# Optimization experiments

Hardware: AMD Instinct MI355X
Metric: run time of the kernel (lower is better)

## Reference

```python
import jax, jax.numpy as jnp
import numpy as np

C = 64
DQ = C // 8  # query/key channel dim


def setup_inputs() -> dict:
    key = jax.random.key(0)
    ks = jax.random.split(key, 8)
    B, H, W = 8, 64, 64
    x = jax.random.normal(ks[0], (B, C, H, W), dtype=jnp.float32)
    # 1x1 conv weights stored as [out, in] matrices (kernel dims squeezed)
    wq = jax.random.normal(ks[1], (DQ, C), dtype=jnp.float32) * 0.05
    bq = jax.random.normal(ks[2], (DQ,), dtype=jnp.float32) * 0.05
    wk = jax.random.normal(ks[3], (DQ, C), dtype=jnp.float32) * 0.05
    bk = jax.random.normal(ks[4], (DQ,), dtype=jnp.float32) * 0.05
    wv = jax.random.normal(ks[5], (C, C), dtype=jnp.float32) * 0.05
    bv = jax.random.normal(ks[6], (C,), dtype=jnp.float32) * 0.05
    gamma = jax.random.normal(ks[7], (1,), dtype=jnp.float32)
    return {"x": x, "wq": wq, "bq": bq, "wk": wk, "bk": bk,
            "wv": wv, "bv": bv, "gamma": gamma}


def reference(x, wq, bq, wk, bk, wv, bv, gamma):
    B, Cc, H, W = x.shape
    N = H * W
    xf = x.reshape(B, Cc, N)                      # [B, C, N]
    # 1x1 convs == channel matmuls
    q = jnp.einsum('dc,bcn->bdn', wq, xf) + bq[None, :, None]   # [B, DQ, N]
    k = jnp.einsum('dc,bcn->bdn', wk, xf) + bk[None, :, None]   # [B, DQ, N]
    v = jnp.einsum('oc,bcn->bon', wv, xf) + bv[None, :, None]   # [B, C, N]
    # energy[b, m, n] = sum_d q[b, d, m] * k[b, d, n]
    energy = jnp.einsum('bdm,bdn->bmn', q, k)                   # [B, N, N]
    attention = jax.nn.softmax(energy, axis=-1)
    # out[b, c, m] = sum_n v[b, c, n] * attention[b, m, n]
    out = jnp.einsum('bcn,bmn->bcm', v, attention).reshape(B, Cc, H, W)
    return gamma[0] * out + x
```

## Files before the change

kernel.cpp:

```cpp
#include <hip/hip_runtime.h>
#include <math.h>

#define NTOK 4096
#define CCH  64
#define LOG2E 1.4426950408889634f

typedef __attribute__((ext_vector_type(8)))  short bf16x8;
typedef __attribute__((ext_vector_type(4)))  float f32x4;
typedef __attribute__((ext_vector_type(16))) float f32x16;
typedef __attribute__((ext_vector_type(2)))  unsigned int uint32x2;

__device__ __forceinline__ unsigned short f2bf_rne(float f) {
    unsigned int u = __float_as_uint(f);
    u += 0x7FFFu + ((u >> 16) & 1u);
    return (unsigned short)(u >> 16);
}
__device__ __forceinline__ unsigned short f2bf_trunc(float f) {
    return (unsigned short)(__float_as_uint(f) >> 16);
}
__device__ __forceinline__ float bf2f(unsigned short u) {
    return __uint_as_float(((unsigned int)u) << 16);
}

__global__ __launch_bounds__(256) void proj_kernel(
    const float* __restrict__ x,
    const float* __restrict__ wq, const float* __restrict__ bq,
    const float* __restrict__ wk, const float* __restrict__ bk,
    const float* __restrict__ wv, const float* __restrict__ bv,
    unsigned short* __restrict__ qt, unsigned short* __restrict__ kt,
    unsigned short* __restrict__ vbf)
{
    __shared__ unsigned short xsb[64 * 68];
    __shared__ unsigned short wa[80 * 68];
    __shared__ unsigned short vtmp[64 * 66];
    __shared__ float bb[80];

    const int t  = threadIdx.x;
    const int b  = blockIdx.x >> 6;
    const int n0 = (blockIdx.x & 63) << 6;

    const int lane = t & 63;
    const int w    = t >> 6;
    const int l15  = lane & 15;
    const int g    = lane >> 4;

    {
        const int n  = t & 63;
        const int c0 = t >> 6;
        #pragma unroll
        for (int r = 0; r < 16; ++r) {
            const int c = c0 + 4 * r;
            xsb[n * 68 + c] = f2bf_rne(x[((size_t)(b * CCH + c)) * NTOK + n0 + n]);
        }
    }
    #pragma unroll
    for (int r = 0; r < 16; ++r) {
        const int i = t + 256 * r;
        wa[(i >> 6) * 68 + (i & 63)] = f2bf_rne(wv[i]);
    }
    {
        const int i0 = t, i1 = t + 256;
        wa[(64 + (i0 >> 6)) * 68 + (i0 & 63)] = f2bf_rne(wq[i0] * LOG2E);
        wa[(64 + (i1 >> 6)) * 68 + (i1 & 63)] = f2bf_rne(wq[i1] * LOG2E);
        wa[(72 + (i0 >> 6)) * 68 + (i0 & 63)] = f2bf_rne(wk[i0]);
        wa[(72 + (i1 >> 6)) * 68 + (i1 & 63)] = f2bf_rne(wk[i1]);
    }
    if (t < 80) {
        float bias;
        if (t < 64)      bias = bv[t];
        else if (t < 72) bias = bq[t - 64] * LOG2E;
        else             bias = bk[t - 72];
        bb[t] = bias;
    }
    __syncthreads();

    f32x4 acc[5];
    #pragma unroll
    for (int mt = 0; mt < 5; ++mt) acc[mt] = (f32x4){0.f, 0.f, 0.f, 0.f};
    #pragma unroll
    for (int kc = 0; kc < 2; ++kc) {
        const bf16x8 bx = *(const bf16x8*)&xsb[(w * 16 + l15) * 68 + kc * 32 + g * 8];
        #pragma unroll
        for (int mt = 0; mt < 5; ++mt) {
            const bf16x8 aw = *(const bf16x8*)&wa[(mt * 16 + l15) * 68 + kc * 32 + g * 8];
            acc[mt] = __builtin_amdgcn_mfma_f32_16x16x32_bf16(aw, bx, acc[mt], 0, 0, 0);
        }
    }

    const int n = w * 16 + l15;
    #pragma unroll
    for (int mt = 0; mt < 4; ++mt) {
        #pragma unroll
        for (int r = 0; r < 4; ++r) {
            const int c = mt * 16 + g * 4 + r;
            vtmp[c * 66 + 4 * l15 + w] = f2bf_rne(acc[mt][r] + bb[c]);
        }
    }
    {
        unsigned short vals[4];
        #pragma unroll
        for (int r = 0; r < 4; ++r)
            vals[r] = f2bf_rne(acc[4][r] + bb[64 + g * 4 + r]);
        const unsigned int lo = (unsigned int)vals[0] | ((unsigned int)vals[1] << 16);
        const unsigned int hi = (unsigned int)vals[2] | ((unsigned int)vals[3] << 16);
        unsigned short* dst = ((g < 2) ? qt : kt) +
                              ((size_t)(b * NTOK + n0 + n)) * 8 + (g & 1) * 4;
        *(uint32x2*)dst = (uint32x2){lo, hi};
    }
    __syncthreads();

    {
        const int c = t >> 2;
        const int q = t & 3;
        unsigned short* dst = vbf + ((size_t)(b * CCH + c)) * NTOK + n0 + q * 16;
        *(bf16x8*)dst       = *(const bf16x8*)&vtmp[c * 66 + q * 16];
        *(bf16x8*)(dst + 8) = *(const bf16x8*)&vtmp[c * 66 + q * 16 + 8];
    }
}

__global__ __launch_bounds__(256, 4) void attn_kernel(
    const unsigned short* __restrict__ qt, const unsigned short* __restrict__ kt,
    const unsigned short* __restrict__ vbf,
    unsigned short* __restrict__ opart, float* __restrict__ lpart)
{
    __shared__ unsigned short qs[64 * 32];
    __shared__ unsigned short ks[64 * 40];
    __shared__ unsigned short vs[64 * 88];
    __shared__ unsigned short ps[64 * 88];

    const int t    = threadIdx.x;
    const int lane = t & 63;
    const int w    = t >> 6;
    const int p    = blockIdx.x >> 9;
    const int rest = blockIdx.x & 511;
    const int b    = rest >> 6;
    const int m0   = (rest & 63) << 6;

    const int l15 = lane & 15;
    const int g   = lane >> 4;
    const int l31 = lane & 31;
    const int h   = lane >> 5;

    if (t < 64) {
        *(bf16x8*)&qs[t * 32] = *(const bf16x8*)&qt[((size_t)(b * NTOK + m0 + t)) * 8];
        bf16x8 z = {};
        *(bf16x8*)&qs[t * 32 + 8]  = z;
        *(bf16x8*)&qs[t * 32 + 16] = z;
        *(bf16x8*)&qs[t * 32 + 24] = z;
        *(bf16x8*)&ks[t * 40 + 8]  = z;
        *(bf16x8*)&ks[t * 40 + 16] = z;
        *(bf16x8*)&ks[t * 40 + 24] = z;
    }
    __syncthreads();

    const bf16x8 a_q = *(const bf16x8*)&qs[(w * 16 + l15) * 32 + g * 8];

    f32x16 oacc;
    #pragma unroll
    for (int i = 0; i < 16; ++i) oacc[i] = 0.f;
    float rs0 = 0.f, rs1 = 0.f, rs2 = 0.f, rs3 = 0.f;

    const int crow = ((w >> 1) * 32 + l31) * 88;
    const int mrow = ((w & 1) * 32 + l31) * 88;

    for (int it = p * 32; it < p * 32 + 32; ++it) {
        const int nt0 = it << 6;
        __syncthreads();

        if (t < 64)
            *(bf16x8*)&ks[t * 40] = *(const bf16x8*)&kt[((size_t)(b * NTOK + nt0 + t)) * 8];
        #pragma unroll
        for (int r = 0; r < 2; ++r) {
            const int i   = t + 256 * r;
            const int c   = i >> 3;
            const int seg = i & 7;
            *(bf16x8*)&vs[c * 88 + seg * 8] =
                *(const bf16x8*)&vbf[((size_t)(b * CCH + c)) * NTOK + nt0 + seg * 8];
        }
        __syncthreads();

        f32x4 s0, s1, s2, s3;
        {
            const bf16x8 bk0 = *(const bf16x8*)&ks[( 0 + l15) * 40 + g * 8];
            const bf16x8 bk1 = *(const bf16x8*)&ks[(16 + l15) * 40 + g * 8];
            const bf16x8 bk2 = *(const bf16x8*)&ks[(32 + l15) * 40 + g * 8];
            const bf16x8 bk3 = *(const bf16x8*)&ks[(48 + l15) * 40 + g * 8];
            const f32x4 z = {0.f, 0.f, 0.f, 0.f};
            s0 = __builtin_amdgcn_mfma_f32_16x16x32_bf16(a_q, bk0, z, 0, 0, 0);
            s1 = __builtin_amdgcn_mfma_f32_16x16x32_bf16(a_q, bk1, z, 0, 0, 0);
            s2 = __builtin_amdgcn_mfma_f32_16x16x32_bf16(a_q, bk2, z, 0, 0, 0);
            s3 = __builtin_amdgcn_mfma_f32_16x16x32_bf16(a_q, bk3, z, 0, 0, 0);
        }

        #pragma unroll
        for (int r = 0; r < 4; ++r) {
            const float p0 = exp2f(s0[r]);
            const float p1 = exp2f(s1[r]);
            const float p2 = exp2f(s2[r]);
            const float p3 = exp2f(s3[r]);
            const unsigned int lo = (unsigned int)f2bf_trunc(p0) |
                                    ((unsigned int)f2bf_trunc(p1) << 16);
            const unsigned int hi = (unsigned int)f2bf_trunc(p2) |
                                    ((unsigned int)f2bf_trunc(p3) << 16);
            *(uint32x2*)&ps[(w * 16 + g * 4 + r) * 88 + 4 * l15] = (uint32x2){lo, hi};
            const float ssum = (p0 + p1) + (p2 + p3);
            if      (r == 0) rs0 += ssum;
            else if (r == 1) rs1 += ssum;
            else if (r == 2) rs2 += ssum;
            else             rs3 += ssum;
        }
        __syncthreads();

        #pragma unroll
        for (int kc = 0; kc < 4; ++kc) {
            const bf16x8 a_v = *(const bf16x8*)&vs[crow + kc * 16 + h * 8];
            const bf16x8 b_p = *(const bf16x8*)&ps[mrow + kc * 16 + h * 8];
            oacc = __builtin_amdgcn_mfma_f32_32x32x16_bf16(a_v, b_p, oacc, 0, 0, 0);
        }
    }

    #pragma unroll
    for (int xm = 1; xm <= 8; xm <<= 1) {
        rs0 += __shfl_xor(rs0, xm);
        rs1 += __shfl_xor(rs1, xm);
        rs2 += __shfl_xor(rs2, xm);
        rs3 += __shfl_xor(rs3, xm);
    }
    if (l15 == 0) {
        float* lp = lpart + (size_t)(p * 8 + b) * NTOK + m0 + w * 16 + g * 4;
        lp[0] = rs0; lp[1] = rs1; lp[2] = rs2; lp[3] = rs3;
    }

    {
        const int mloc = (w & 1) * 32 + l31;
        #pragma unroll
        for (int reg = 0; reg < 16; ++reg) {
            const int c = (w >> 1) * 32 + (reg & 3) + 8 * (reg >> 2) + 4 * h;
            opart[((size_t)((p * 8 + b) * CCH + c)) * NTOK + m0 + mloc] =
                f2bf_rne(oacc[reg]);
        }
    }
}

__global__ __launch_bounds__(256) void combine_kernel(
    const unsigned short* __restrict__ opart, const float* __restrict__ lpart,
    const float* __restrict__ x, const float* __restrict__ gamma_p,
    float* __restrict__ out)
{
    const size_t idx = (size_t)blockIdx.x * 256 + threadIdx.x;
    const int m4 = ((int)idx & 1023) * 4;
    const int bc = (int)(idx >> 10);
    const int bi = bc >> 6;

    const size_t obase   = (size_t)bc * NTOK + m4;
    const size_t ostride = (size_t)8 * CCH * NTOK;

    const ushort4 o1 = *(const ushort4*)&opart[obase];
    const ushort4 o2 = *(const ushort4*)&opart[obase + ostride];
    const float4  l1 = *(const float4*)&lpart[(size_t)bi * NTOK + m4];
    const float4  l2 = *(const float4*)&lpart[(size_t)(8 + bi) * NTOK + m4];
    const float4  xv = *(const float4*)&x[obase];
    const float   gm = gamma_p[0];

    float4 r;
    r.x = (bf2f(o1.x) + bf2f(o2.x)) * gm / (l1.x + l2.x) + xv.x;
    r.y = (bf2f(o1.y) + bf2f(o2.y)) * gm / (l1.y + l2.y) + xv.y;
    r.z = (bf2f(o1.z) + bf2f(o2.z)) * gm / (l1.z + l2.z) + xv.z;
    r.w = (bf2f(o1.w) + bf2f(o2.w)) * gm / (l1.w + l2.w) + xv.w;
    *(float4*)&out[obase] = r;
}

extern "C" void kernel_launch(void* const* d_in, const int* in_sizes, int n_in,
                              void* d_out, int out_size, void* d_ws, size_t ws_size,
                              hipStream_t stream) {
    const float* x     = (const float*)d_in[0];
    const float* wq    = (const float*)d_in[1];
    const float* bq    = (const float*)d_in[2];
    const float* wk    = (const float*)d_in[3];
    const float* bk    = (const float*)d_in[4];
    const float* wv    = (const float*)d_in[5];
    const float* bv    = (const float*)d_in[6];
    const float* gamma = (const float*)d_in[7];
    float* out = (float*)d_out;

    const int B = in_sizes[0] / (CCH * NTOK);

    unsigned short* wsp   = (unsigned short*)d_ws;
    unsigned short* qt    = wsp;
    unsigned short* kt    = qt + (size_t)B * NTOK * 8;
    unsigned short* vbf   = kt + (size_t)B * NTOK * 8;
    unsigned short* opart = vbf + (size_t)B * CCH * NTOK;
    float*          lpart = (float*)(opart + (size_t)2 * B * CCH * NTOK);

    proj_kernel<<<B * (NTOK / 64), 256, 0, stream>>>(x, wq, bq, wk, bk, wv, bv,
                                                     qt, kt, vbf);
    attn_kernel<<<2 * B * (NTOK / 64), 256, 0, stream>>>(qt, kt, vbf, opart, lpart);
    combine_kernel<<<(B * CCH * NTOK) / (256 * 4), 256, 0, stream>>>(
        opart, lpart, x, gamma, out);
}
```

Before: 135.7 us.

## Fuse projection, attention and combine into one cooperative persistent kernel

Merges the three kernels into one cooperative launch. Blocks loop over projection tiles, attention tiles and combine elements, with grid.sync between the phases, and the two shared-memory layouts are unioned. The goal is to remove the launch overhead and inter-kernel gaps between the three stages. In exchange it adds host-side occupancy queries on every call, grid-wide barriers, and a grid capped by occupancy, so attention tiles may run in uneven waves. It falls back to the three separate kernels if the cooperative launch fails.

After: 445.9 us. 3.29x slower.

```diff
diff --git a/kernel.cpp b/kernel.cpp
--- a/kernel.cpp
+++ b/kernel.cpp
@@ -1,5 +1,8 @@
 #include <hip/hip_runtime.h>
+#include <hip/hip_cooperative_groups.h>
 #include <math.h>
+
+namespace cg = cooperative_groups;
 
 #define NTOK 4096
 #define CCH  64
@@ -22,7 +25,21 @@
     return __uint_as_float(((unsigned int)u) << 16);
 }
 
-__global__ __launch_bounds__(256) void proj_kernel(
+struct ProjS {
+    unsigned short xsb[64 * 68];
+    unsigned short wa[80 * 68];
+    unsigned short vtmp[64 * 66];
+    float bb[80];
+};
+struct AttnS {
+    unsigned short qs[64 * 32];
+    unsigned short ks[64 * 40];
+    unsigned short vs[64 * 88];
+    unsigned short ps[64 * 88];
+};
+
+__device__ __forceinline__ void proj_tile(
+    ProjS& s, int vb, int t,
     const float* __restrict__ x,
     const float* __restrict__ wq, const float* __restrict__ bq,
     const float* __restrict__ wk, const float* __restrict__ bk,
@@ -30,15 +47,8 @@
     unsigned short* __restrict__ qt, unsigned short* __restrict__ kt,
     unsigned short* __restrict__ vbf)
 {
-    __shared__ unsigned short xsb[64 * 68];
-    __shared__ unsigned short wa[80 * 68];
-    __shared__ unsigned short vtmp[64 * 66];
-    __shared__ float bb[80];
-
-    const int t  = threadIdx.x;
-    const int b  = blockIdx.x >> 6;
-    const int n0 = (blockIdx.x & 63) << 6;
-
+    const int b  = vb >> 6;
+    const int n0 = (vb & 63) << 6;
     const int lane = t & 63;
     const int w    = t >> 6;
     const int l15  = lane & 15;
@@ -50,27 +60,27 @@
         #pragma unroll
         for (int r = 0; r < 16; ++r) {
             const int c = c0 + 4 * r;
-            xsb[n * 68 + c] = f2bf_rne(x[((size_t)(b * CCH + c)) * NTOK + n0 + n]);
+            s.xsb[n * 68 + c] = f2bf_rne(x[((size_t)(b * CCH + c)) * NTOK + n0 + n]);
         }
     }
     #pragma unroll
     for (int r = 0; r < 16; ++r) {
         const int i = t + 256 * r;
-        wa[(i >> 6) * 68 + (i & 63)] = f2bf_rne(wv[i]);
+        s.wa[(i >> 6) * 68 + (i & 63)] = f2bf_rne(wv[i]);
     }
     {
         const int i0 = t, i1 = t + 256;
-        wa[(64 + (i0 >> 6)) * 68 + (i0 & 63)] = f2bf_rne(wq[i0] * LOG2E);
-        wa[(64 + (i1 >> 6)) * 68 + (i1 & 63)] = f2bf_rne(wq[i1] * LOG2E);
-        wa[(72 + (i0 >> 6)) * 68 + (i0 & 63)] = f2bf_rne(wk[i0]);
-        wa[(72 + (i1 >> 6)) * 68 + (i1 & 63)] = f2bf_rne(wk[i1]);
+        s.wa[(64 + (i0 >> 6)) * 68 + (i0 & 63)] = f2bf_rne(wq[i0] * LOG2E);
+        s.wa[(64 + (i1 >> 6)) * 68 + (i1 & 63)] = f2bf_rne(wq[i1] * LOG2E);
+        s.wa[(72 + (i0 >> 6)) * 68 + (i0 & 63)] = f2bf_rne(wk[i0]);
+        s.wa[(72 + (i1 >> 6)) * 68 + (i1 & 63)] = f2bf_rne(wk[i1]);
     }
     if (t < 80) {
         float bias;
         if (t < 64)      bias = bv[t];
         else if (t < 72) bias = bq[t - 64] * LOG2E;
         else             bias = bk[t - 72];
-        bb[t] = bias;
+        s.bb[t] = bias;
     }
     __syncthreads();
 
@@ -79,10 +89,10 @@
     for (int mt = 0; mt < 5; ++mt) acc[mt] = (f32x4){0.f, 0.f, 0.f, 0.f};
     #pragma unroll
     for (int kc = 0; kc < 2; ++kc) {
-        const bf16x8 bx = *(const bf16x8*)&xsb[(w * 16 + l15) * 68 + kc * 32 + g * 8];
+        const bf16x8 bx = *(const bf16x8*)&s.xsb[(w * 16 + l15) * 68 + kc * 32 + g * 8];
         #pragma unroll
         for (int mt = 0; mt < 5; ++mt) {
-            const bf16x8 aw = *(const bf16x8*)&wa[(mt * 16 + l15) * 68 + kc * 32 + g * 8];
+            const bf16x8 aw = *(const bf16x8*)&s.wa[(mt * 16 + l15) * 68 + kc * 32 + g * 8];
             acc[mt] = __builtin_amdgcn_mfma_f32_16x16x32_bf16(aw, bx, acc[mt], 0, 0, 0);
         }
     }
@@ -93,14 +103,14 @@
         #pragma unroll
         for (int r = 0; r < 4; ++r) {
             const int c = mt * 16 + g * 4 + r;
-            vtmp[c * 66 + 4 * l15 + w] = f2bf_rne(acc[mt][r] + bb[c]);
+            s.vtmp[c * 66 + 4 * l15 + w] = f2bf_rne(acc[mt][r] + s.bb[c]);
         }
     }
     {
         unsigned short vals[4];
         #pragma unroll
         for (int r = 0; r < 4; ++r)
-            vals[r] = f2bf_rne(acc[4][r] + bb[64 + g * 4 + r]);
+            vals[r] = f2bf_rne(acc[4][r] + s.bb[64 + g * 4 + r]);
         const unsigned int lo = (unsigned int)vals[0] | ((unsigned int)vals[1] << 16);
         const unsigned int hi = (unsigned int)vals[2] | ((unsigned int)vals[3] << 16);
         unsigned short* dst = ((g < 2) ? qt : kt) +
@@ -113,47 +123,42 @@
         const int c = t >> 2;
         const int q = t & 3;
         unsigned short* dst = vbf + ((size_t)(b * CCH + c)) * NTOK + n0 + q * 16;
-        *(bf16x8*)dst       = *(const bf16x8*)&vtmp[c * 66 + q * 16];
-        *(bf16x8*)(dst + 8) = *(const bf16x8*)&vtmp[c * 66 + q * 16 + 8];
-    }
-}
-
-__global__ __launch_bounds__(256, 4) void attn_kernel(
+        *(bf16x8*)dst       = *(const bf16x8*)&s.vtmp[c * 66 + q * 16];
+        *(bf16x8*)(dst + 8) = *(const bf16x8*)&s.vtmp[c * 66 + q * 16 + 8];
+    }
+}
+
+__device__ __forceinline__ void attn_tile(
+    AttnS& s, int vb, int t, int B,
     const unsigned short* __restrict__ qt, const unsigned short* __restrict__ kt,
     const unsigned short* __restrict__ vbf,
     unsigned short* __restrict__ opart, float* __restrict__ lpart)
 {
-    __shared__ unsigned short qs[64 * 32];
-    __shared__ unsigned short ks[64 * 40];
-    __shared__ unsigned short vs[64 * 88];
-    __shared__ unsigned short ps[64 * 88];
-
-    const int t    = threadIdx.x;
+    const int p    = vb / (B * 64);
+    const int rest = vb % (B * 64);
+    const int b    = rest >> 6;
+    const int m0   = (rest & 63) << 6;
+
     const int lane = t & 63;
     const int w    = t >> 6;
-    const int p    = blockIdx.x >> 9;
-    const int rest = blockIdx.x & 511;
-    const int b    = rest >> 6;
-    const int m0   = (rest & 63) << 6;
-
-    const int l15 = lane & 15;
-    const int g   = lane >> 4;
-    const int l31 = lane & 31;
-    const int h   = lane >> 5;
+    const int l15  = lane & 15;
+    const int g    = lane >> 4;
+    const int l31  = lane & 31;
+    const int h    = lane >> 5;
 
     if (t < 64) {
-        *(bf16x8*)&qs[t * 32] = *(const bf16x8*)&qt[((size_t)(b * NTOK + m0 + t)) * 8];
+        *(bf16x8*)&s.qs[t * 32] = *(const bf16x8*)&qt[((size_t)(b * NTOK + m0 + t)) * 8];
         bf16x8 z = {};
-        *(bf16x8*)&qs[t * 32 + 8]  = z;
-        *(bf16x8*)&qs[t * 32 + 16] = z;
-        *(bf16x8*)&qs[t * 32 + 24] = z;
-        *(bf16x8*)&ks[t * 40 + 8]  = z;
-        *(bf16x8*)&ks[t * 40 + 16] = z;
-        *(bf16x8*)&ks[t * 40 + 24] = z;
+        *(bf16x8*)&s.qs[t * 32 + 8]  = z;
+        *(bf16x8*)&s.qs[t * 32 + 16] = z;
+        *(bf16x8*)&s.qs[t * 32 + 24] = z;
+        *(bf16x8*)&s.ks[t * 40 + 8]  = z;
+        *(bf16x8*)&s.ks[t * 40 + 16] = z;
+        *(bf16x8*)&s.ks[t * 40 + 24] = z;
     }
     __syncthreads();
 
-    const bf16x8 a_q = *(const bf16x8*)&qs[(w * 16 + l15) * 32 + g * 8];
+    const bf16x8 a_q = *(const bf16x8*)&s.qs[(w * 16 + l15) * 32 + g * 8];
 
     f32x16 oacc;
     #pragma unroll
@@ -168,23 +173,24 @@
         __syncthreads();
 
         if (t < 64)
-            *(bf16x8*)&ks[t * 40] = *(const bf16x8*)&kt[((size_t)(b * NTOK + nt0 + t)) * 8];
+            *(bf16x8*)&s.ks[t * 40] =
+                *(const bf16x8*)&kt[((size_t)(b * NTOK + nt0 + t)) * 8];
         #pragma unroll
         for (int r = 0; r < 2; ++r) {
             const int i   = t + 256 * r;
             const int c   = i >> 3;
             const int seg = i & 7;
-            *(bf16x8*)&vs[c * 88 + seg * 8] =
+            *(bf16x8*)&s.vs[c * 88 + seg * 8] =
                 *(const bf16x8*)&vbf[((size_t)(b * CCH + c)) * NTOK + nt0 + seg * 8];
         }
         __syncthreads();
 
         f32x4 s0, s1, s2, s3;
         {
-            const bf16x8 bk0 = *(const bf16x8*)&ks[( 0 + l15) * 40 + g * 8];
-            const bf16x8 bk1 = *(const bf16x8*)&ks[(16 + l15) * 40 + g * 8];
-            const bf16x8 bk2 = *(const bf16x8*)&ks[(32 + l15) * 40 + g * 8];
-            const bf16x8 bk3 = *(const bf16x8*)&ks[(48 + l15) * 40 + g * 8];
+            const bf16x8 bk0 = *(const bf16x8*)&s.ks[( 0 + l15) * 40 + g * 8];
+            const bf16x8 bk1 = *(const bf16x8*)&s.ks[(16 + l15) * 40 + g * 8];
+            const bf16x8 bk2 = *(const bf16x8*)&s.ks[(32 + l15) * 40 + g * 8];
+            const bf16x8 bk3 = *(const bf16x8*)&s.ks[(48 + l15) * 40 + g * 8];
             const f32x4 z = {0.f, 0.f, 0.f, 0.f};
             s0 = __builtin_amdgcn_mfma_f32_16x16x32_bf16(a_q, bk0, z, 0, 0, 0);
             s1 = __builtin_amdgcn_mfma_f32_16x16x32_bf16(a_q, bk1, z, 0, 0, 0);
@@ -202,7 +208,7 @@
                                     ((unsigned int)f2bf_trunc(p1) << 16);
             const unsigned int hi = (unsigned int)f2bf_trunc(p2) |
                                     ((unsigned int)f2bf_trunc(p3) << 16);
-            *(uint32x2*)&ps[(w * 16 + g * 4 + r) * 88 + 4 * l15] = (uint32x2){lo, hi};
+            *(uint32x2*)&s.ps[(w * 16 + g * 4 + r) * 88 + 4 * l15] = (uint32x2){lo, hi};
             const float ssum = (p0 + p1) + (p2 + p3);
             if      (r == 0) rs0 += ssum;
             else if (r == 1) rs1 += ssum;
@@ -213,8 +219,8 @@
 
         #pragma unroll
         for (int kc = 0; kc < 4; ++kc) {
-            const bf16x8 a_v = *(const bf16x8*)&vs[crow + kc * 16 + h * 8];
-            const bf16x8 b_p = *(const bf16x8*)&ps[mrow + kc * 16 + h * 8];
+            const bf16x8 a_v = *(const bf16x8*)&s.vs[crow + kc * 16 + h * 8];
+            const bf16x8 b_p = *(const bf16x8*)&s.ps[mrow + kc * 16 + h * 8];
             oacc = __builtin_amdgcn_mfma_f32_32x32x16_bf16(a_v, b_p, oacc, 0, 0, 0);
         }
     }
@@ -227,47 +233,106 @@
         rs3 += __shfl_xor(rs3, xm);
     }
     if (l15 == 0) {
-        float* lp = lpart + (size_t)(p * 8 + b) * NTOK + m0 + w * 16 + g * 4;
+        float* lp = lpart + (size_t)(p * B + b) * NTOK + m0 + w * 16 + g * 4;
         lp[0] = rs0; lp[1] = rs1; lp[2] = rs2; lp[3] = rs3;
     }
-
     {
         const int mloc = (w & 1) * 32 + l31;
         #pragma unroll
         for (int reg = 0; reg < 16; ++reg) {
             const int c = (w >> 1) * 32 + (reg & 3) + 8 * (reg >> 2) + 4 * h;
-            opart[((size_t)((p * 8 + b) * CCH + c)) * NTOK + m0 + mloc] =
+            opart[((size_t)((p * B + b) * CCH + c)) * NTOK + m0 + mloc] =
                 f2bf_rne(oacc[reg]);
         }
     }
+}
+
+__device__ __forceinline__ void combine_span(
+    int t, int nblocks, int blockid, int B,
+    const unsigned short* __restrict__ opart, const float* __restrict__ lpart,
+    const float* __restrict__ x, const float* __restrict__ gamma_p,
+    float* __restrict__ out)
+{
+    const float  gm      = gamma_p[0];
+    const size_t nf4     = (size_t)B * CCH * NTOK / 4;
+    const size_t ostride = (size_t)B * CCH * NTOK;
+    for (size_t f = (size_t)blockid * 256 + t; f < nf4; f += (size_t)nblocks * 256) {
+        const int m4 = ((int)(f & 1023)) * 4;
+        const int bc = (int)(f >> 10);
+        const int bi = bc >> 6;
+        const size_t obase = (size_t)bc * NTOK + m4;
+
+        const ushort4 o1 = *(const ushort4*)&opart[obase];
+        const ushort4 o2 = *(const ushort4*)&opart[obase + ostride];
+        const float4  l1 = *(const float4*)&lpart[(size_t)bi * NTOK + m4];
+        const float4  l2 = *(const float4*)&lpart[(size_t)(B + bi) * NTOK + m4];
+        const float4  xv = *(const float4*)&x[obase];
+
+        float4 r;
+        r.x = (bf2f(o1.x) + bf2f(o2.x)) * gm / (l1.x + l2.x) + xv.x;
+        r.y = (bf2f(o1.y) + bf2f(o2.y)) * gm / (l1.y + l2.y) + xv.y;
+        r.z = (bf2f(o1.z) + bf2f(o2.z)) * gm / (l1.z + l2.z) + xv.z;
+        r.w = (bf2f(o1.w) + bf2f(o2.w)) * gm / (l1.w + l2.w) + xv.w;
+        *(float4*)&out[obase] = r;
+    }
+}
+
+__global__ __launch_bounds__(256, 4) void fused_kernel(
+    const float* __restrict__ x,
+    const float* __restrict__ wq, const float* __restrict__ bq,
+    const float* __restrict__ wk, const float* __restrict__ bk,
+    const float* __restrict__ wv, const float* __restrict__ bv,
+    const float* __restrict__ gamma_p, float* __restrict__ out,
+    unsigned short* __restrict__ qt, unsigned short* __restrict__ kt,
+    unsigned short* __restrict__ vbf,
+    unsigned short* __restrict__ opart, float* __restrict__ lpart, int B)
+{
+    __shared__ union { ProjS p; AttnS a; } sm;
+    cg::grid_group grid = cg::this_grid();
+    const int t = threadIdx.x;
+
+    for (int vb = blockIdx.x; vb < B * 64; vb += gridDim.x) {
+        __syncthreads();
+        proj_tile(sm.p, vb, t, x, wq, bq, wk, bk, wv, bv, qt, kt, vbf);
+    }
+    __threadfence();
+    grid.sync();
+
+    for (int vb = blockIdx.x; vb < 2 * B * 64; vb += gridDim.x)
+        attn_tile(sm.a, vb, t, B, qt, kt, vbf, opart, lpart);
+    __threadfence();
+    grid.sync();
+
+    combine_span(t, gridDim.x, blockIdx.x, B, opart, lpart, x, gamma_p, out);
+}
+
+__global__ __launch_bounds__(256) void proj_kernel(
+    const float* __restrict__ x,
+    const float* __restrict__ wq, const float* __restrict__ bq,
+    const float* __restrict__ wk, const float* __restrict__ bk,
+    const float* __restrict__ wv, const float* __restrict__ bv,
+    unsigned short* __restrict__ qt, unsigned short* __restrict__ kt,
+    unsigned short* __restrict__ vbf)
+{
+    __shared__ ProjS s;
+    proj_tile(s, blockIdx.x, threadIdx.x, x, wq, bq, wk, bk, wv, bv, qt, kt, vbf);
+}
+
+__global__ __launch_bounds__(256, 4) void attn_kernel(
+    const unsigned short* __restrict__ qt, const unsigned short* __restrict__ kt,
+    const unsigned short* __restrict__ vbf,
+    unsigned short* __restrict__ opart, float* __restrict__ lpart, int B)
+{
+    __shared__ AttnS s;
+    attn_tile(s, blockIdx.x, threadIdx.x, B, qt, kt, vbf, opart, lpart);
 }
 
 __global__ __launch_bounds__(256) void combine_kernel(
     const unsigned short* __restrict__ opart, const float* __restrict__ lpart,
     const float* __restrict__ x, const float* __restrict__ gamma_p,
-    float* __restrict__ out)
-{
-    const size_t idx = (size_t)blockIdx.x * 256 + threadIdx.x;
-    const int m4 = ((int)idx & 1023) * 4;
-    const int bc = (int)(idx >> 10);
-    const int bi = bc >> 6;
-
-    const size_t obase   = (size_t)bc * NTOK + m4;
-    const size_t ostride = (size_t)8 * CCH * NTOK;
-
-    const ushort4 o1 = *(const ushort4*)&opart[obase];
-    const ushort4 o2 = *(const ushort4*)&opart[obase + ostride];
-    const float4  l1 = *(const float4*)&lpart[(size_t)bi * NTOK + m4];
-    const float4  l2 = *(const float4*)&lpart[(size_t)(8 + bi) * NTOK + m4];
-    const float4  xv = *(const float4*)&x[obase];
-    const float   gm = gamma_p[0];
-
-    float4 r;
-    r.x = (bf2f(o1.x) + bf2f(o2.x)) * gm / (l1.x + l2.x) + xv.x;
-    r.y = (bf2f(o1.y) + bf2f(o2.y)) * gm / (l1.y + l2.y) + xv.y;
-    r.z = (bf2f(o1.z) + bf2f(o2.z)) * gm / (l1.z + l2.z) + xv.z;
-    r.w = (bf2f(o1.w) + bf2f(o2.w)) * gm / (l1.w + l2.w) + xv.w;
-    *(float4*)&out[obase] = r;
+    float* __restrict__ out, int B)
+{
+    combine_span(threadIdx.x, gridDim.x, blockIdx.x, B, opart, lpart, x, gamma_p, out);
 }
 
 extern "C" void kernel_launch(void* const* d_in, const int* in_sizes, int n_in,
@@ -283,7 +348,7 @@
     const float* gamma = (const float*)d_in[7];
     float* out = (float*)d_out;
 
-    const int B = in_sizes[0] / (CCH * NTOK);
+    int B = in_sizes[0] / (CCH * NTOK);
 
     unsigned short* wsp   = (unsigned short*)d_ws;
     unsigned short* qt    = wsp;
@@ -292,9 +357,37 @@
     unsigned short* opart = vbf + (size_t)B * CCH * NTOK;
     float*          lpart = (float*)(opart + (size_t)2 * B * CCH * NTOK);
 
-    proj_kernel<<<B * (NTOK / 64), 256, 0, stream>>>(x, wq, bq, wk, bk, wv, bv,
-                                                     qt, kt, vbf);
-    attn_kernel<<<2 * B * (NTOK / 64), 256, 0, stream>>>(qt, kt, vbf, opart, lpart);
-    combine_kernel<<<(B * CCH * NTOK) / (256 * 4), 256, 0, stream>>>(
-        opart, lpart, x, gamma, out);
-}
+    int dev = 0;
+    (void)hipGetDevice(&dev);
+    int numCU = 0;
+    (void)hipDeviceGetAttribute(&numCU, hipDeviceAttributeMultiprocessorCount, dev);
+    int perCU = 0;
+    hipError_t qerr = hipOccupancyMaxActiveBlocksPerMultiprocessor(
+        &perCU, (const void*)fused_kernel, 256, 0);
+
+    const int want = 2 * B * 64;
+    int grid = 0;
+    if (qerr == hipSuccess && perCU > 0 && numCU > 0) {
+        grid = perCU * numCU;
+        if (grid > want) grid = want;
+    }
+
+    hipError_t lerr = hipErrorUnknown;
+    if (grid >= 64) {
+        void* args[] = {
+            (void*)&x,  (void*)&wq, (void*)&bq, (void*)&wk, (void*)&bk,
+            (void*)&wv, (void*)&bv, (void*)&gamma, (void*)&out,
+            (void*)&qt, (void*)&kt, (void*)&vbf, (void*)&opart, (void*)&lpart,
+            (void*)&B
+        };
+        lerr = hipLaunchCooperativeKernel((const void*)fused_kernel, dim3(grid),
+                                          dim3(256), args, 0, stream);
+    }
+    if (lerr != hipSuccess) {
+        (void)hipGetLastError();
+        proj_kernel<<<B * 64, 256, 0, stream>>>(x, wq, bq, wk, bk, wv, bv,
+                                                qt, kt, vbf);
+        attn_kernel<<<2 * B * 64, 256, 0, stream>>>(qt, kt, vbf, opart, lpart, B);
+        combine_kernel<<<256, 256, 0, stream>>>(opart, lpart, x, gamma, out, B);
+    }
+}
```

## Fuse split-K combine into attention kernel via atomic ticket, use perm for bf16 pack

Applied to the files above, without the earlier changes.

The separate combine kernel is removed. Each of the two split blocks increments an atomic ticket after writing its partials, and the second block to finish merges both partials, normalizes, applies gamma and adds the residual. This saves one kernel launch and lets the combine overlap with other blocks' attention work, at the cost of a threadfence, an extra memset launch for the tickets, and a serial tail inside the last block. The bf16 truncation packing is also replaced with a single byte-permute instruction.

Result: slower. 269.0 us (+98.2%).

```diff
diff --git a/kernel.cpp b/kernel.cpp
--- a/kernel.cpp
+++ b/kernel.cpp
@@ -14,9 +14,6 @@
     unsigned int u = __float_as_uint(f);
     u += 0x7FFFu + ((u >> 16) & 1u);
     return (unsigned short)(u >> 16);
-}
-__device__ __forceinline__ unsigned short f2bf_trunc(float f) {
-    return (unsigned short)(__float_as_uint(f) >> 16);
 }
 __device__ __forceinline__ float bf2f(unsigned short u) {
     return __uint_as_float(((unsigned int)u) << 16);
@@ -121,18 +118,22 @@
 __global__ __launch_bounds__(256, 4) void attn_kernel(
     const unsigned short* __restrict__ qt, const unsigned short* __restrict__ kt,
     const unsigned short* __restrict__ vbf,
-    unsigned short* __restrict__ opart, float* __restrict__ lpart)
+    unsigned short* __restrict__ opart, float* __restrict__ lpart,
+    int* __restrict__ tickets,
+    const float* __restrict__ x, const float* __restrict__ gamma_p,
+    float* __restrict__ out, int B)
 {
     __shared__ unsigned short qs[64 * 32];
     __shared__ unsigned short ks[64 * 40];
     __shared__ unsigned short vs[64 * 88];
     __shared__ unsigned short ps[64 * 88];
+    __shared__ int do_comb;
 
     const int t    = threadIdx.x;
     const int lane = t & 63;
     const int w    = t >> 6;
-    const int p    = blockIdx.x >> 9;
-    const int rest = blockIdx.x & 511;
+    const int p    = blockIdx.x / (B * 64);
+    const int rest = blockIdx.x % (B * 64);
     const int b    = rest >> 6;
     const int m0   = (rest & 63) << 6;
 
@@ -168,7 +169,8 @@
         __syncthreads();
 
         if (t < 64)
-            *(bf16x8*)&ks[t * 40] = *(const bf16x8*)&kt[((size_t)(b * NTOK + nt0 + t)) * 8];
+            *(bf16x8*)&ks[t * 40] =
+                *(const bf16x8*)&kt[((size_t)(b * NTOK + nt0 + t)) * 8];
         #pragma unroll
         for (int r = 0; r < 2; ++r) {
             const int i   = t + 256 * r;
@@ -198,10 +200,10 @@
             const float p1 = exp2f(s1[r]);
             const float p2 = exp2f(s2[r]);
             const float p3 = exp2f(s3[r]);
-            const unsigned int lo = (unsigned int)f2bf_trunc(p0) |
-                                    ((unsigned int)f2bf_trunc(p1) << 16);
-            const unsigned int hi = (unsigned int)f2bf_trunc(p2) |
-                                    ((unsigned int)f2bf_trunc(p3) << 16);
+            const unsigned int lo = __builtin_amdgcn_perm(
+                __float_as_uint(p1), __float_as_uint(p0), 0x07060302u);
+            const unsigned int hi = __builtin_amdgcn_perm(
+                __float_as_uint(p3), __float_as_uint(p2), 0x07060302u);
             *(uint32x2*)&ps[(w * 16 + g * 4 + r) * 88 + 4 * l15] = (uint32x2){lo, hi};
             const float ssum = (p0 + p1) + (p2 + p3);
             if      (r == 0) rs0 += ssum;
@@ -227,47 +229,48 @@
         rs3 += __shfl_xor(rs3, xm);
     }
     if (l15 == 0) {
-        float* lp = lpart + (size_t)(p * 8 + b) * NTOK + m0 + w * 16 + g * 4;
+        float* lp = lpart + (size_t)(p * B + b) * NTOK + m0 + w * 16 + g * 4;
         lp[0] = rs0; lp[1] = rs1; lp[2] = rs2; lp[3] = rs3;
     }
-
     {
         const int mloc = (w & 1) * 32 + l31;
         #pragma unroll
         for (int reg = 0; reg < 16; ++reg) {
             const int c = (w >> 1) * 32 + (reg & 3) + 8 * (reg >> 2) + 4 * h;
-            opart[((size_t)((p * 8 + b) * CCH + c)) * NTOK + m0 + mloc] =
+            opart[((size_t)((p * B + b) * CCH + c)) * NTOK + m0 + mloc] =
                 f2bf_rne(oacc[reg]);
         }
     }
-}
-
-__global__ __launch_bounds__(256) void combine_kernel(
-    const unsigned short* __restrict__ opart, const float* __restrict__ lpart,
-    const float* __restrict__ x, const float* __restrict__ gamma_p,
-    float* __restrict__ out)
-{
-    const size_t idx = (size_t)blockIdx.x * 256 + threadIdx.x;
-    const int m4 = ((int)idx & 1023) * 4;
-    const int bc = (int)(idx >> 10);
-    const int bi = bc >> 6;
-
-    const size_t obase   = (size_t)bc * NTOK + m4;
-    const size_t ostride = (size_t)8 * CCH * NTOK;
-
-    const ushort4 o1 = *(const ushort4*)&opart[obase];
-    const ushort4 o2 = *(const ushort4*)&opart[obase + ostride];
-    const float4  l1 = *(const float4*)&lpart[(size_t)bi * NTOK + m4];
-    const float4  l2 = *(const float4*)&lpart[(size_t)(8 + bi) * NTOK + m4];
-    const float4  xv = *(const float4*)&x[obase];
-    const float   gm = gamma_p[0];
-
-    float4 r;
-    r.x = (bf2f(o1.x) + bf2f(o2.x)) * gm / (l1.x + l2.x) + xv.x;
-    r.y = (bf2f(o1.y) + bf2f(o2.y)) * gm / (l1.y + l2.y) + xv.y;
-    r.z = (bf2f(o1.z) + bf2f(o2.z)) * gm / (l1.z + l2.z) + xv.z;
-    r.w = (bf2f(o1.w) + bf2f(o2.w)) * gm / (l1.w + l2.w) + xv.w;
-    *(float4*)&out[obase] = r;
+
+    __threadfence();
+    __syncthreads();
+    if (t == 0)
+        do_comb = (atomicAdd(&tickets[rest], 1) == 1);
+    __syncthreads();
+    if (do_comb) {
+        __threadfence();
+        const float  gm      = gamma_p[0];
+        const size_t ostride = (size_t)B * CCH * NTOK;
+        const int c   = t >> 2;
+        const int ms0 = (t & 3) * 16;
+        const size_t base = (size_t)(b * CCH + c) * NTOK + m0 + ms0;
+        #pragma unroll
+        for (int j = 0; j < 4; ++j) {
+            const size_t obase = base + j * 4;
+            const int    mm    = ms0 + j * 4;
+            const ushort4 o1 = *(const ushort4*)&opart[obase];
+            const ushort4 o2 = *(const ushort4*)&opart[obase + ostride];
+            const float4  l1 = *(const float4*)&lpart[(size_t)b * NTOK + m0 + mm];
+            const float4  l2 = *(const float4*)&lpart[(size_t)(B + b) * NTOK + m0 + mm];
+            const float4  xv = *(const float4*)&x[obase];
+            float4 r;
+            r.x = (bf2f(o1.x) + bf2f(o2.x)) * gm / (l1.x + l2.x) + xv.x;
+            r.y = (bf2f(o1.y) + bf2f(o2.y)) * gm / (l1.y + l2.y) + xv.y;
+            r.z = (bf2f(o1.z) + bf2f(o2.z)) * gm / (l1.z + l2.z) + xv.z;
+            r.w = (bf2f(o1.w) + bf2f(o2.w)) * gm / (l1.w + l2.w) + xv.w;
+            *(float4*)&out[obase] = r;
+        }
+    }
 }
 
 extern "C" void kernel_launch(void* const* d_in, const int* in_sizes, int n_in,
@@ -283,18 +286,19 @@
     const float* gamma = (const float*)d_in[7];
     float* out = (float*)d_out;
 
-    const int B = in_sizes[0] / (CCH * NTOK);
-
-    unsigned short* wsp   = (unsigned short*)d_ws;
-    unsigned short* qt    = wsp;
-    unsigned short* kt    = qt + (size_t)B * NTOK * 8;
-    unsigned short* vbf   = kt + (size_t)B * NTOK * 8;
-    unsigned short* opart = vbf + (size_t)B * CCH * NTOK;
-    float*          lpart = (float*)(opart + (size_t)2 * B * CCH * NTOK);
-
-    proj_kernel<<<B * (NTOK / 64), 256, 0, stream>>>(x, wq, bq, wk, bk, wv, bv,
-                                                     qt, kt, vbf);
-    attn_kernel<<<2 * B * (NTOK / 64), 256, 0, stream>>>(qt, kt, vbf, opart, lpart);
-    combine_kernel<<<(B * CCH * NTOK) / (256 * 4), 256, 0, stream>>>(
-        opart, lpart, x, gamma, out);
-}
+    int B = in_sizes[0] / (CCH * NTOK);
+
+    unsigned short* wsp     = (unsigned short*)d_ws;
+    unsigned short* qt      = wsp;
+    unsigned short* kt      = qt + (size_t)B * NTOK * 8;
+    unsigned short* vbf     = kt + (size_t)B * NTOK * 8;
+    unsigned short* opart   = vbf + (size_t)B * CCH * NTOK;
+    float*          lpart   = (float*)(opart + (size_t)2 * B * CCH * NTOK);
+    int*            tickets = (int*)(lpart + (size_t)2 * B * NTOK);
+
+    hipMemsetAsync(tickets, 0, (size_t)B * 64 * sizeof(int), stream);
+
+    proj_kernel<<<B * 64, 256, 0, stream>>>(x, wq, bq, wk, bk, wv, bv, qt, kt, vbf);
+    attn_kernel<<<2 * B * 64, 256, 0, stream>>>(qt, kt, vbf, opart, lpart,
+                                                tickets, x, gamma, out, B);
+}
```
